# Optimization experiments

Hardware: AMD Instinct MI355X
Metric: run time of the kernel (lower is better)

Reference implementation:

```python
import jax, jax.numpy as jnp
import numpy as np

MUL0, MUL1 = 128, 64            # scalar (0e) and vector (1o) multiplicities
B = 8192                        # batch of nodes
SQRT3 = 3.0 ** 0.5
SQRT6 = 6.0 ** 0.5

# path normalization (e3nn 'component' irrep norm / 'element' path norm):
# coeff_ins = sqrt(dim(ir_out) / fan_in(i_out)), fan_in = sum_{ins -> i_out} mul1*mul2
A_0E = (1.0 / (MUL0 * MUL0 + MUL1 * MUL1)) ** 0.5   # paths (0,0,0)+(1,1,0)
A_1O = (3.0 / (MUL0 * MUL1 + MUL1 * MUL0)) ** 0.5   # paths (0,1,1)+(1,0,1)
A_1E = (3.0 / (MUL1 * MUL1)) ** 0.5                  # path  (1,1,1)


def _levi_civita():
    eps = np.zeros((3, 3, 3), dtype=np.float32)
    eps[0, 1, 2] = eps[1, 2, 0] = eps[2, 0, 1] = 1.0
    eps[0, 2, 1] = eps[2, 1, 0] = eps[1, 0, 2] = -1.0
    return jnp.asarray(eps)


def setup_inputs() -> dict:
    key = jax.random.key(0)
    ks = jax.random.split(key, 7)
    return {
        "x1": jax.random.normal(ks[0], (B, MUL0 + 3 * MUL1), dtype=jnp.float32),
        "x2": jax.random.normal(ks[1], (B, MUL0 + 3 * MUL1), dtype=jnp.float32),
        "w000": jax.random.normal(ks[2], (MUL0, MUL0, MUL0), dtype=jnp.float32),
        "w011": jax.random.normal(ks[3], (MUL0, MUL1, MUL1), dtype=jnp.float32),
        "w101": jax.random.normal(ks[4], (MUL1, MUL0, MUL1), dtype=jnp.float32),
        "w110": jax.random.normal(ks[5], (MUL1, MUL1, MUL0), dtype=jnp.float32),
        "w111": jax.random.normal(ks[6], (MUL1, MUL1, MUL1), dtype=jnp.float32),
    }


def reference(x1, x2, w000, w011, w101, w110, w111):
    b = x1.shape[0]
    # split irreps: scalars [b, 128], vectors [b, 64, 3]
    s1, v1 = x1[:, :MUL0], x1[:, MUL0:].reshape(b, MUL1, 3)
    s2, v2 = x2[:, :MUL0], x2[:, MUL0:].reshape(b, MUL1, 3)

    # 0e output: 0e x 0e -> 0e (w3j = 1) and 1o x 1o -> 0e (w3j = delta/sqrt3)
    out0 = A_0E * (
        jnp.einsum("uvw,bu,bv->bw", w000, s1, s2)
        + jnp.einsum("uvw,bui,bvi->bw", w110, v1, v2) / SQRT3
    )

    # 1o output: 0e x 1o -> 1o and 1o x 0e -> 1o (w3j = delta/sqrt3)
    out1o = (A_1O / SQRT3) * (
        jnp.einsum("uvw,bu,bvi->bwi", w011, s1, v2)
        + jnp.einsum("uvw,bui,bv->bwi", w101, v1, s2)
    )

    # 1e output: 1o x 1o -> 1e (w3j = levi-civita / sqrt6)
    eps = _levi_civita()
    out1e = (A_1E / SQRT6) * jnp.einsum("uvw,bui,bvj,ijk->bwk", w111, v1, v2, eps)

    return jnp.concatenate(
        [out0, out1o.reshape(b, -1), out1e.reshape(b, -1)], axis=-1
    )  # [b, 128 + 192 + 192] = [b, 512]
```

## Files before the change

kernel.cpp:

```cpp
#include <hip/hip_runtime.h>
#include <stdint.h>


typedef _Float16 f16;
typedef f16 f16x8 __attribute__((ext_vector_type(8)));
typedef float f32x4 __attribute__((ext_vector_type(4)));
typedef int i32x4 __attribute__((ext_vector_type(4)));

#define OFF_W000 0u
#define OFF_W110 2097152u
#define OFF_W011 2621440u
#define OFF_W101 3145728u
#define OFF_W111 3670016u
#define OFF_XS1  3932160u
#define OFF_XS2  4980736u
#define OFF_XV1  6029312u
#define OFF_XV2  7602176u
#define OFF_S0A  9175040u
#define OFF_S0B  10223616u
#define OFF_S1O  13369344u
#define WS_ELEMS 14942208u

#define SC_0E 0.006987712429686843f
#define SC_1O 0.0078125f
#define SC_1E 0.011048543456039806f

__global__ void tile_all_k(const float* __restrict__ w000, const float* __restrict__ w011,
                           const float* __restrict__ w101, const float* __restrict__ w110,
                           const float* __restrict__ w111, const float* __restrict__ x1,
                           const float* __restrict__ x2, f16* __restrict__ ws)
{
  unsigned tid = blockIdx.x*256u + threadIdx.x;
  if (tid < 2097152u) {
    unsigned e=tid&7u, n=(tid>>3)&63u, q=(tid>>9)&3u, p=(tid>>11)&1u,
             u=(tid>>12)&127u, vh=(tid>>19)&1u, h=(tid>>20)&1u;
    unsigned v = vh*64u + p*32u + q*8u + e;
    ws[OFF_W000+tid] = (f16)w000[u*16384u + v*128u + h*64u + n];
    return;
  }
  tid -= 2097152u;
  if (tid < 524288u) {
    unsigned e=tid&7u, n=(tid>>3)&63u, q=(tid>>9)&3u, p=(tid>>11)&1u,
             u=(tid>>12)&63u, h=(tid>>18)&1u;
    unsigned v = p*32u + q*8u + e;
    ws[OFF_W110+tid] = (f16)(w110[u*8192u + v*128u + h*64u + n] * 0.5773502691896258f);
    return;
  }
  tid -= 524288u;
  if (tid < 524288u) {
    unsigned e=tid&7u, n=(tid>>3)&63u, q=(tid>>9)&3u, p=(tid>>11)&1u, u=tid>>12;
    unsigned v = p*32u + q*8u + e;
    ws[OFF_W011+tid] = (f16)w011[u*4096u + v*64u + n];
    return;
  }
  tid -= 524288u;
  if (tid < 524288u) {
    unsigned e=tid&7u, n=(tid>>3)&63u, q=(tid>>9)&3u, p=(tid>>11)&1u, u=tid>>12;
    unsigned v = p*32u + q*8u + e;
    ws[OFF_W101+tid] = (f16)w101[v*8192u + u*64u + n];
    return;
  }
  tid -= 524288u;
  if (tid < 262144u) {
    unsigned e=tid&7u, n=(tid>>3)&63u, q=(tid>>9)&3u, p=(tid>>11)&1u, u=tid>>12;
    unsigned v = p*32u + q*8u + e;
    ws[OFF_W111+tid] = (f16)w111[u*4096u + v*64u + n];
    return;
  }
  tid -= 262144u;
  if (tid < 1048576u) {
    unsigned e=tid&7u, r=(tid>>3)&127u, uo=(tid>>10)&15u, rt=tid>>14;
    ws[OFF_XS1+tid] = (f16)x1[(rt*128u+r)*320u + uo*8u + e];
    return;
  }
  tid -= 1048576u;
  if (tid < 1572864u) {
    unsigned e=tid&7u, r=(tid>>3)&127u, ov=(tid>>10)&7u, rest=tid>>13;
    unsigned i=rest%3u, rt=rest/3u;
    ws[OFF_XV1+tid] = (f16)x1[(rt*128u+r)*320u + 128u + (ov*8u+e)*3u + i];
    return;
  }
  tid -= 1572864u;
  if (tid < 1048576u) {
    unsigned e=tid&7u, r=(tid>>3)&127u, uo=(tid>>10)&15u, rt=tid>>14;
    ws[OFF_XS2+tid] = (f16)x2[(rt*128u+r)*320u + uo*8u + e];
    return;
  }
  tid -= 1048576u;
  {
    unsigned e=tid&7u, r=(tid>>3)&127u, ov=(tid>>10)&7u, rest=tid>>13;
    unsigned i=rest%3u, rt=rest/3u;
    ws[OFF_XV2+tid] = (f16)x2[(rt*128u+r)*320u + 128u + (ov*8u+e)*3u + i];
  }
}

#define GLD16(g,l) __builtin_amdgcn_global_load_lds( \
    (const __attribute__((address_space(1))) unsigned int*)(g), \
    (__attribute__((address_space(3))) unsigned int*)(l), 16, 0, 0)

#define WAITV(n) asm volatile("s_waitcnt vmcnt(" #n ")" ::: "memory")

template<bool NEG, int SS>
__device__ __forceinline__ void run_phase(const f16* __restrict__ Wt,
    const f16* __restrict__ aW, const f16* __restrict__ bW, int bRow,
    f16* sWw, f16* sAw, f32x4 (&acc)[4][4], int lane)
{
  constexpr int M = SS*8;
  const int q = lane >> 4, r15 = lane & 15;

  f16x8 br[4][2];
#pragma unroll
  for (int mt=0; mt<4; ++mt)
#pragma unroll
    for (int o=0; o<2; ++o)
      br[mt][o] = *(const f16x8*)(bW + (o*4+q)*1024 + (bRow + mt*16 + r15)*8);
#pragma unroll
  for (int mt=0; mt<4; ++mt)
#pragma unroll
    for (int o=0; o<2; ++o) {
      i32x4 tmp = __builtin_bit_cast(i32x4, br[mt][o]);
      asm volatile("" :: "v"(tmp));
    }

  auto stPair = [&](int p, int slot){
    const char* s = (const char*)Wt + (size_t)p*8192;
    char* d = (char*)sWw + slot*8192;
#pragma unroll
    for (int c=0; c<8; ++c)
      GLD16(s + c*1024 + lane*16, d + c*1024);
  };
  auto stA = [&](int ss2){
    GLD16((const char*)(aW + ss2*1024) + lane*16, (char*)sAw + (ss2&1)*1024);
  };

  stPair(0,0); stA(0); stPair(1,1);

  f16x8 aR[4];
#pragma unroll 1
  for (int ss = 0; ss < SS; ++ss) {
#pragma unroll
    for (int kc = 0; kc < 8; ++kc) {
      const int t = ss*8 + kc;
      if (kc == 7) { if (ss+1 < SS) { WAITV(9); } else { WAITV(0); } }
      else         { WAITV(8); }
      if (kc == 0) {
#pragma unroll
        for (int mt=0; mt<4; ++mt)
          aR[mt] = *(const f16x8*)(sAw + (ss&1)*512 + (mt*16+r15)*8);
      }
      __builtin_amdgcn_s_setprio(1);
#pragma unroll
      for (int p=0; p<2; ++p) {
        f16x8 af[4];
#pragma unroll
        for (int mt=0; mt<4; ++mt) {
          f16 av = aR[mt][kc];
          if constexpr (NEG) av = -av;
          af[mt] = av * br[mt][p];
        }
#pragma unroll
        for (int nt=0; nt<4; ++nt) {
          f16x8 bw = *(const f16x8*)(sWw + (kc&1)*4096 + p*2048 + (q*64 + nt*16 + r15)*8);
#pragma unroll
          for (int mt=0; mt<4; ++mt)
            acc[mt][nt] = __builtin_amdgcn_mfma_f32_16x16x32_f16(af[mt], bw, acc[mt][nt], 0,0,0);
        }
      }
      __builtin_amdgcn_s_setprio(0);
      __builtin_amdgcn_sched_barrier(0);
      if (kc == 6 && ss+1 < SS) stA(ss+1);
      if (t + 2 < M) stPair(t+2, kc&1);
    }
  }
}

__global__ __launch_bounds__(256, 2)
void tp_main(f16* __restrict__ ws, float* __restrict__ out)
{
  __shared__ f16 smem[36864];
  const int lane = threadIdx.x & 63, wid = threadIdx.x >> 6;
  f16* sWw = smem + wid*8192;
  f16* sAw = smem + 32768 + wid*1024;
  const int q = lane >> 4, r15 = lane & 15;
  const int sub = wid >> 1, rh = wid & 1;

  f32x4 acc[4][4];
#pragma unroll
  for (int a=0;a<4;++a)
#pragma unroll
    for (int b=0;b<4;++b) acc[a][b] = (f32x4){0.f,0.f,0.f,0.f};

  const int bid = blockIdx.x;

#define STORE_DIRECT(base_col_expr, SC)                                   \
  _Pragma("unroll")                                                       \
  for (int mt=0;mt<4;++mt)                                                \
    _Pragma("unroll")                                                     \
    for (int nt=0;nt<4;++nt)                                              \
      _Pragma("unroll")                                                   \
      for (int rg=0;rg<4;++rg)                                            \
        out[(rowb+mt*16+q*4+rg)*512 + (base_col_expr)] = (SC)*acc[mt][nt][rg];

#define STORE_SLAB(slab, stride, col_expr, SC)                            \
  _Pragma("unroll")                                                       \
  for (int mt=0;mt<4;++mt)                                                \
    _Pragma("unroll")                                                     \
    for (int nt=0;nt<4;++nt)                                              \
      _Pragma("unroll")                                                   \
      for (int rg=0;rg<4;++rg)                                            \
        (slab)[(rowb+mt*16+q*4+rg)*(stride) + (col_expr)] = (f16)((SC)*acc[mt][nt][rg]);

  if (bid < 128) {
    const int rtp = bid >> 2, vh = (bid >> 1) & 1, h = bid & 1;
    const int rtt = rtp*2 + sub;
    const f16* aW = ws + OFF_XS1 + rtt*16384 + rh*512;
    const f16* bW = ws + OFF_XS2 + rtt*16384 + vh*8192;
    const f16* Wt = ws + OFF_W000 + h*1048576u + vh*524288u;
    run_phase<false,16>(Wt, aW, bW, rh*64, sWw, sAw, acc, lane);
    const int rowb = rtt*128 + rh*64;
    if (vh == 0) { STORE_DIRECT(h*64+nt*16+r15, SC_0E) }
    else { f16* slab = ws + OFF_S0A; STORE_SLAB(slab, 128, h*64+nt*16+r15, SC_0E) }
  } else if (bid < 224) {
    const int id = bid-128, i = id%3, rtp = id/3;
    const int rtt = rtp*2 + sub;
    const f16* aW = ws + OFF_XS1 + rtt*16384 + rh*512;
    const f16* bW = ws + OFF_XV2 + (rtt*3+i)*8192;
    run_phase<false,16>(ws + OFF_W011, aW, bW, rh*64, sWw, sAw, acc, lane);
    const int rowb = rtt*128 + rh*64;
    STORE_DIRECT(128 + 3*(nt*16+r15) + i, SC_1O)
  } else if (bid < 320) {
    const int id = bid-224, i = id%3, rtp = id/3;
    const int rtt = rtp*2 + sub;
    const f16* aW = ws + OFF_XS2 + rtt*16384 + rh*512;
    const f16* bW = ws + OFF_XV1 + (rtt*3+i)*8192;
    run_phase<false,16>(ws + OFF_W101, aW, bW, rh*64, sWw, sAw, acc, lane);
    const int rowb = rtt*128 + rh*64;
    f16* slab = ws + OFF_S1O;
    STORE_SLAB(slab, 192, 3*(nt*16+r15) + i, SC_1O)
  } else if (bid < 416) {
    const int id = bid-320, kk = id%3, rtp = id/3;
    int i = kk+1; if (i>2) i-=3;
    int j = kk+2; if (j>2) j-=3;
    const int rtt = rtp*2 + sub;
    run_phase<false,8>(ws + OFF_W111,
        ws + OFF_XV1 + (rtt*3+i)*8192 + rh*512, ws + OFF_XV2 + (rtt*3+j)*8192,
        rh*64, sWw, sAw, acc, lane);
    run_phase<true,8>(ws + OFF_W111,
        ws + OFF_XV1 + (rtt*3+j)*8192 + rh*512, ws + OFF_XV2 + (rtt*3+i)*8192,
        rh*64, sWw, sAw, acc, lane);
    const int rowb = rtt*128 + rh*64;
    STORE_DIRECT(320 + 3*(nt*16+r15) + kk, SC_1E)
  } else {
    const int id = bid-416, i = id%3, h = (id/3)&1, rtp = id/6;
    const int rtt = rtp*2 + sub;
    const f16* aW = ws + OFF_XV1 + (rtt*3+i)*8192 + rh*512;
    const f16* bW = ws + OFF_XV2 + (rtt*3+i)*8192;
    run_phase<false,8>(ws + OFF_W110 + h*262144u, aW, bW, rh*64, sWw, sAw, acc, lane);
    const int rowb = rtt*128 + rh*64;
    f16* slab = ws + OFF_S0B + (unsigned)i*1048576u;
    STORE_SLAB(slab, 128, h*64+nt*16+r15, SC_0E)
  }
#undef STORE_DIRECT
#undef STORE_SLAB
}

__global__ void ep_add(const f16* __restrict__ ws, float* __restrict__ out)
{
  unsigned tid = blockIdx.x*256u + threadIdx.x;
  if (tid < 1048576u) {
    unsigned r = tid>>7, c = tid&127u;
    float s = (float)ws[OFF_S0A+tid] + (float)ws[OFF_S0B+tid]
            + (float)ws[OFF_S0B+1048576u+tid] + (float)ws[OFF_S0B+2097152u+tid];
    out[r*512u+c] += s;
  } else {
    unsigned t2 = tid - 1048576u;
    unsigned r = t2/192u, c = t2 - r*192u;
    out[r*512u+128u+c] += (float)ws[OFF_S1O+t2];
  }
}

extern "C" void kernel_launch(void* const* d_in, const int* in_sizes, int n_in,
                              void* d_out, int out_size, void* d_ws, size_t ws_size,
                              hipStream_t stream)
{
  const float* x1   = (const float*)d_in[0];
  const float* x2   = (const float*)d_in[1];
  const float* w000 = (const float*)d_in[2];
  const float* w011 = (const float*)d_in[3];
  const float* w101 = (const float*)d_in[4];
  const float* w110 = (const float*)d_in[5];
  const float* w111 = (const float*)d_in[6];
  float* out = (float*)d_out;
  f16* ws   = (f16*)d_ws;

  if (ws_size < (size_t)WS_ELEMS * 2) return;

  tile_all_k<<<35840, 256, 0, stream>>>(w000, w011, w101, w110, w111, x1, x2, ws);
  tp_main<<<608, 256, 0, stream>>>(ws, out);
  ep_add<<<10240, 256, 0, stream>>>(ws, out);
}
```

Baseline: 157.6 us.

## Share weight tiles across waves in LDS and split N across waves

Before, each wave streamed its own private copy of the weight tile into LDS. Now the four waves of a block load a shared weight tile cooperatively, with each wave staging a quarter of it and using a 4-slot ring with block barriers. Each block now covers one 128-row tile, with waves split by row half and N half, and the accumulators shrink to 4x2. Lower LDS and register use allows 4 blocks per CU, and the grid grows to 1024 blocks with a remapped job order. In exchange this adds a workgroup barrier every k-step and halves per-wave reuse of the A fragments.

```diff
diff --git a/kernel.cpp b/kernel.cpp
--- a/kernel.cpp
+++ b/kernel.cpp
@@ -102,11 +102,13 @@
 
 template<bool NEG, int SS>
 __device__ __forceinline__ void run_phase(const f16* __restrict__ Wt,
-    const f16* __restrict__ aW, const f16* __restrict__ bW, int bRow,
-    f16* sWw, f16* sAw, f32x4 (&acc)[4][4], int lane)
+    const f16* __restrict__ aW, const f16* __restrict__ bW, int bRow, int nh,
+    f16* sW, f16* sAw, f32x4 (&acc)[4][2], int lane, int wid)
 {
   constexpr int M = SS*8;
   const int q = lane >> 4, r15 = lane & 15;
+
+  WAITV(0);
 
   f16x8 br[4][2];
 #pragma unroll
@@ -123,17 +125,16 @@
     }
 
   auto stPair = [&](int p, int slot){
-    const char* s = (const char*)Wt + (size_t)p*8192;
-    char* d = (char*)sWw + slot*8192;
-#pragma unroll
-    for (int c=0; c<8; ++c)
-      GLD16(s + c*1024 + lane*16, d + c*1024);
+    const char* s = (const char*)Wt + p*8192 + wid*2048 + lane*16;
+    char* d = (char*)sW + slot*8192 + wid*2048;
+    GLD16(s, d);
+    GLD16(s + 1024, d + 1024);
   };
   auto stA = [&](int ss2){
     GLD16((const char*)(aW + ss2*1024) + lane*16, (char*)sAw + (ss2&1)*1024);
   };
 
-  stPair(0,0); stA(0); stPair(1,1);
+  stA(0); stPair(0,0); stPair(1,1); stPair(2,2);
 
   f16x8 aR[4];
 #pragma unroll 1
@@ -141,8 +142,13 @@
 #pragma unroll
     for (int kc = 0; kc < 8; ++kc) {
       const int t = ss*8 + kc;
-      if (kc == 7) { if (ss+1 < SS) { WAITV(9); } else { WAITV(0); } }
-      else         { WAITV(8); }
+      if (kc == 7)      { if (ss+1 < SS) { WAITV(5); } else { WAITV(0); } }
+      else if (kc == 6) { if (ss+1 < SS) { WAITV(4); } else { WAITV(2); } }
+      else              { WAITV(4); }
+      __builtin_amdgcn_s_barrier();
+      __builtin_amdgcn_sched_barrier(0);
+      if (kc == 6 && ss+1 < SS) stA(ss+1);
+      if (t + 3 < M) stPair(t+3, (kc+3)&3);
       if (kc == 0) {
 #pragma unroll
         for (int mt=0; mt<4; ++mt)
@@ -159,106 +165,110 @@
           af[mt] = av * br[mt][p];
         }
 #pragma unroll
-        for (int nt=0; nt<4; ++nt) {
-          f16x8 bw = *(const f16x8*)(sWw + (kc&1)*4096 + p*2048 + (q*64 + nt*16 + r15)*8);
+        for (int nt=0; nt<2; ++nt) {
+          f16x8 bw = *(const f16x8*)(sW + (kc&3)*4096 + p*2048 + q*512
+                                     + (nh*32 + nt*16 + r15)*8);
 #pragma unroll
           for (int mt=0; mt<4; ++mt)
             acc[mt][nt] = __builtin_amdgcn_mfma_f32_16x16x32_f16(af[mt], bw, acc[mt][nt], 0,0,0);
         }
       }
       __builtin_amdgcn_s_setprio(0);
-      __builtin_amdgcn_sched_barrier(0);
-      if (kc == 6 && ss+1 < SS) stA(ss+1);
-      if (t + 2 < M) stPair(t+2, kc&1);
     }
   }
-}
-
-__global__ __launch_bounds__(256, 2)
+  __builtin_amdgcn_s_barrier();
+  __builtin_amdgcn_sched_barrier(0);
+}
+
+__global__ __launch_bounds__(256, 4)
 void tp_main(f16* __restrict__ ws, float* __restrict__ out)
 {
-  __shared__ f16 smem[36864];
+  __shared__ f16 smem[20480];
+  f16* sW = smem;
   const int lane = threadIdx.x & 63, wid = threadIdx.x >> 6;
-  f16* sWw = smem + wid*8192;
-  f16* sAw = smem + 32768 + wid*1024;
+  f16* sAw = smem + 16384 + wid*1024;
   const int q = lane >> 4, r15 = lane & 15;
-  const int sub = wid >> 1, rh = wid & 1;
-
-  f32x4 acc[4][4];
+  const int rh = wid & 1, nh = wid >> 1;
+
+  f32x4 acc[4][2];
 #pragma unroll
   for (int a=0;a<4;++a)
 #pragma unroll
-    for (int b=0;b<4;++b) acc[a][b] = (f32x4){0.f,0.f,0.f,0.f};
-
-  const int bid = blockIdx.x;
-
-#define STORE_DIRECT(base_col_expr, SC)                                   \
+    for (int b=0;b<2;++b) acc[a][b] = (f32x4){0.f,0.f,0.f,0.f};
+
+  const int jid = (blockIdx.x & 7)*128 + (blockIdx.x >> 3);
+
+#define STORE_DIRECT(col_expr, SC)                                        \
   _Pragma("unroll")                                                       \
   for (int mt=0;mt<4;++mt)                                                \
     _Pragma("unroll")                                                     \
-    for (int nt=0;nt<4;++nt)                                              \
+    for (int nt=0;nt<2;++nt)                                              \
       _Pragma("unroll")                                                   \
       for (int rg=0;rg<4;++rg)                                            \
-        out[(rowb+mt*16+q*4+rg)*512 + (base_col_expr)] = (SC)*acc[mt][nt][rg];
+        out[(rowb+mt*16+q*4+rg)*512 + (col_expr)] = (SC)*acc[mt][nt][rg];
 
 #define STORE_SLAB(slab, stride, col_expr, SC)                            \
   _Pragma("unroll")                                                       \
   for (int mt=0;mt<4;++mt)                                                \
     _Pragma("unroll")                                                     \
-    for (int nt=0;nt<4;++nt)                                              \
+    for (int nt=0;nt<2;++nt)                                              \
       _Pragma("unroll")                                                   \
       for (int rg=0;rg<4;++rg)                                            \
         (slab)[(rowb+mt*16+q*4+rg)*(stride) + (col_expr)] = (f16)((SC)*acc[mt][nt][rg]);
 
-  if (bid < 128) {
-    const int rtp = bid >> 2, vh = (bid >> 1) & 1, h = bid & 1;
-    const int rtt = rtp*2 + sub;
-    const f16* aW = ws + OFF_XS1 + rtt*16384 + rh*512;
-    const f16* bW = ws + OFF_XS2 + rtt*16384 + vh*8192;
+  if (jid < 256) {
+    const int quarter = jid >> 6, rt = jid & 63;
+    const int h = quarter & 1, vh = quarter >> 1;
+    const f16* aW = ws + OFF_XS1 + rt*16384 + rh*512;
+    const f16* bW = ws + OFF_XS2 + rt*16384 + vh*8192;
     const f16* Wt = ws + OFF_W000 + h*1048576u + vh*524288u;
-    run_phase<false,16>(Wt, aW, bW, rh*64, sWw, sAw, acc, lane);
-    const int rowb = rtt*128 + rh*64;
-    if (vh == 0) { STORE_DIRECT(h*64+nt*16+r15, SC_0E) }
-    else { f16* slab = ws + OFF_S0A; STORE_SLAB(slab, 128, h*64+nt*16+r15, SC_0E) }
-  } else if (bid < 224) {
-    const int id = bid-128, i = id%3, rtp = id/3;
-    const int rtt = rtp*2 + sub;
-    const f16* aW = ws + OFF_XS1 + rtt*16384 + rh*512;
-    const f16* bW = ws + OFF_XV2 + (rtt*3+i)*8192;
-    run_phase<false,16>(ws + OFF_W011, aW, bW, rh*64, sWw, sAw, acc, lane);
-    const int rowb = rtt*128 + rh*64;
-    STORE_DIRECT(128 + 3*(nt*16+r15) + i, SC_1O)
-  } else if (bid < 320) {
-    const int id = bid-224, i = id%3, rtp = id/3;
-    const int rtt = rtp*2 + sub;
-    const f16* aW = ws + OFF_XS2 + rtt*16384 + rh*512;
-    const f16* bW = ws + OFF_XV1 + (rtt*3+i)*8192;
-    run_phase<false,16>(ws + OFF_W101, aW, bW, rh*64, sWw, sAw, acc, lane);
-    const int rowb = rtt*128 + rh*64;
+    run_phase<false,16>(Wt, aW, bW, rh*64, nh, sW, sAw, acc, lane, wid);
+    const int rowb = rt*128 + rh*64;
+    if (vh == 0) { STORE_DIRECT(h*64 + nh*32 + nt*16 + r15, SC_0E) }
+    else { f16* slab = ws + OFF_S0A; STORE_SLAB(slab, 128, h*64 + nh*32 + nt*16 + r15, SC_0E) }
+  } else if (jid < 448) {
+    const int s = jid-256, i = s>>6, rt = s&63;
+    const f16* aW = ws + OFF_XS1 + rt*16384 + rh*512;
+    const f16* bW = ws + OFF_XV2 + (rt*3+i)*8192;
+    run_phase<false,16>(ws + OFF_W011, aW, bW, rh*64, nh, sW, sAw, acc, lane, wid);
+    const int rowb = rt*128 + rh*64;
+    STORE_DIRECT(128 + 3*(nh*32 + nt*16 + r15) + i, SC_1O)
+  } else if (jid < 640) {
+    const int s = jid-448, i = s>>6, rt = s&63;
+    const f16* aW = ws + OFF_XS2 + rt*16384 + rh*512;
+    const f16* bW = ws + OFF_XV1 + (rt*3+i)*8192;
+    run_phase<false,16>(ws + OFF_W101, aW, bW, rh*64, nh, sW, sAw, acc, lane, wid);
+    const int rowb = rt*128 + rh*64;
     f16* slab = ws + OFF_S1O;
-    STORE_SLAB(slab, 192, 3*(nt*16+r15) + i, SC_1O)
-  } else if (bid < 416) {
-    const int id = bid-320, kk = id%3, rtp = id/3;
+    STORE_SLAB(slab, 192, 3*(nh*32 + nt*16 + r15) + i, SC_1O)
+  } else if (jid < 832) {
+    const int s = jid-640, kk = s>>6, rt = s&63;
     int i = kk+1; if (i>2) i-=3;
     int j = kk+2; if (j>2) j-=3;
-    const int rtt = rtp*2 + sub;
     run_phase<false,8>(ws + OFF_W111,
-        ws + OFF_XV1 + (rtt*3+i)*8192 + rh*512, ws + OFF_XV2 + (rtt*3+j)*8192,
-        rh*64, sWw, sAw, acc, lane);
+        ws + OFF_XV1 + (rt*3+i)*8192 + rh*512, ws + OFF_XV2 + (rt*3+j)*8192,
+        rh*64, nh, sW, sAw, acc, lane, wid);
     run_phase<true,8>(ws + OFF_W111,
-        ws + OFF_XV1 + (rtt*3+j)*8192 + rh*512, ws + OFF_XV2 + (rtt*3+i)*8192,
-        rh*64, sWw, sAw, acc, lane);
-    const int rowb = rtt*128 + rh*64;
-    STORE_DIRECT(320 + 3*(nt*16+r15) + kk, SC_1E)
+        ws + OFF_XV1 + (rt*3+j)*8192 + rh*512, ws + OFF_XV2 + (rt*3+i)*8192,
+        rh*64, nh, sW, sAw, acc, lane, wid);
+    const int rowb = rt*128 + rh*64;
+    STORE_DIRECT(320 + 3*(nh*32 + nt*16 + r15) + kk, SC_1E)
   } else {
-    const int id = bid-416, i = id%3, h = (id/3)&1, rtp = id/6;
-    const int rtt = rtp*2 + sub;
-    const f16* aW = ws + OFF_XV1 + (rtt*3+i)*8192 + rh*512;
-    const f16* bW = ws + OFF_XV2 + (rtt*3+i)*8192;
-    run_phase<false,8>(ws + OFF_W110 + h*262144u, aW, bW, rh*64, sWw, sAw, acc, lane);
-    const int rowb = rtt*128 + rh*64;
+    const int s = jid-832, i = s>>6, rt = s&63;
+    const f16* aW = ws + OFF_XV1 + (rt*3+i)*8192 + rh*512;
+    const f16* bW = ws + OFF_XV2 + (rt*3+i)*8192;
+    const int rowb = rt*128 + rh*64;
     f16* slab = ws + OFF_S0B + (unsigned)i*1048576u;
-    STORE_SLAB(slab, 128, h*64+nt*16+r15, SC_0E)
+#pragma unroll 1
+    for (int h = 0; h < 2; ++h) {
+      run_phase<false,8>(ws + OFF_W110 + (unsigned)h*262144u, aW, bW, rh*64, nh,
+                         sW, sAw, acc, lane, wid);
+      STORE_SLAB(slab, 128, h*64 + nh*32 + nt*16 + r15, SC_0E)
+#pragma unroll
+      for (int a=0;a<4;++a)
+#pragma unroll
+        for (int b=0;b<2;++b) acc[a][b] = (f32x4){0.f,0.f,0.f,0.f};
+    }
   }
 #undef STORE_DIRECT
 #undef STORE_SLAB
@@ -296,6 +306,6 @@
   if (ws_size < (size_t)WS_ELEMS * 2) return;
 
   tile_all_k<<<35840, 256, 0, stream>>>(w000, w011, w101, w110, w111, x1, x2, ws);
-  tp_main<<<608, 256, 0, stream>>>(ws, out);
+  tp_main<<<1024, 256, 0, stream>>>(ws, out);
   ep_add<<<10240, 256, 0, stream>>>(ws, out);
 }
```

Result: slower. 165.0 us (+4.7%).

## Restructure tensor-product GEMMs into single-wave 32x32 MFMA jobs with split-K partials

Applied to the files above, without the earlier changes.

Replaces 4-wave 256-thread blocks running 16x16x32 MFMAs with 2048 single-wavefront blocks using 32x32x16 MFMAs, each computing a 128-row by 64-column tile over a half-K slice. The weight and activation staging layouts are re-tiled to match, with a 4-slot LDS pipeline and more split-K partial slabs. The epilogue becomes a row-major pass that sums up to six f16 partials per output. This aims to raise parallelism and MFMA efficiency and to balance work across CUs, at the cost of a larger workspace, more f16 partial traffic and reduction work in ep_add, and less intra-block reuse.

```diff
diff --git a/kernel.cpp b/kernel.cpp
--- a/kernel.cpp
+++ b/kernel.cpp
@@ -4,7 +4,7 @@
 
 typedef _Float16 f16;
 typedef f16 f16x8 __attribute__((ext_vector_type(8)));
-typedef float f32x4 __attribute__((ext_vector_type(4)));
+typedef float f32x16 __attribute__((ext_vector_type(16)));
 typedef int i32x4 __attribute__((ext_vector_type(4)));
 
 #define OFF_W000 0u
@@ -16,10 +16,10 @@
 #define OFF_XS2  4980736u
 #define OFF_XV1  6029312u
 #define OFF_XV2  7602176u
-#define OFF_S0A  9175040u
-#define OFF_S0B  10223616u
-#define OFF_S1O  13369344u
-#define WS_ELEMS 14942208u
+#define OFF_S0   9175040u
+#define OFF_S1   15466496u
+#define OFF_S2   20185088u
+#define WS_ELEMS 21757952u
 
 #define SC_0E 0.006987712429686843f
 #define SC_1O 0.0078125f
@@ -32,65 +32,77 @@
 {
   unsigned tid = blockIdx.x*256u + threadIdx.x;
   if (tid < 2097152u) {
-    unsigned e=tid&7u, n=(tid>>3)&63u, q=(tid>>9)&3u, p=(tid>>11)&1u,
-             u=(tid>>12)&127u, vh=(tid>>19)&1u, h=(tid>>20)&1u;
-    unsigned v = vh*64u + p*32u + q*8u + e;
-    ws[OFF_W000+tid] = (f16)w000[u*16384u + v*128u + h*64u + n];
+    unsigned e=tid&7u, col=(tid>>3)&31u, hf=(tid>>8)&1u, kk=(tid>>9)&1u,
+             ct=(tid>>10)&1u, t=(tid>>11)&127u, q=tid>>18;
+    unsigned h=q&1u, uh=(q>>1)&1u, vh=q>>2;
+    unsigned u = uh*64u + (t>>1);
+    unsigned v = vh*64u + (t&1u)*32u + kk*16u + hf*8u + e;
+    unsigned n = h*64u + ct*32u + col;
+    ws[OFF_W000+tid] = (f16)w000[u*16384u + v*128u + n];
     return;
   }
   tid -= 2097152u;
   if (tid < 524288u) {
-    unsigned e=tid&7u, n=(tid>>3)&63u, q=(tid>>9)&3u, p=(tid>>11)&1u,
-             u=(tid>>12)&63u, h=(tid>>18)&1u;
-    unsigned v = p*32u + q*8u + e;
-    ws[OFF_W110+tid] = (f16)(w110[u*8192u + v*128u + h*64u + n] * 0.5773502691896258f);
+    unsigned e=tid&7u, col=(tid>>3)&31u, hf=(tid>>8)&1u, kk=(tid>>9)&1u,
+             ct=(tid>>10)&1u, t=(tid>>11)&127u, h=tid>>18;
+    unsigned u = t>>1;
+    unsigned v = (t&1u)*32u + kk*16u + hf*8u + e;
+    unsigned n = h*64u + ct*32u + col;
+    ws[OFF_W110+tid] = (f16)(w110[u*8192u + v*128u + n] * 0.5773502691896258f);
     return;
   }
   tid -= 524288u;
   if (tid < 524288u) {
-    unsigned e=tid&7u, n=(tid>>3)&63u, q=(tid>>9)&3u, p=(tid>>11)&1u, u=tid>>12;
-    unsigned v = p*32u + q*8u + e;
+    unsigned e=tid&7u, col=(tid>>3)&31u, hf=(tid>>8)&1u, kk=(tid>>9)&1u,
+             ct=(tid>>10)&1u, t=(tid>>11)&127u, uh=tid>>18;
+    unsigned u = uh*64u + (t>>1);
+    unsigned v = (t&1u)*32u + kk*16u + hf*8u + e;
+    unsigned n = ct*32u + col;
     ws[OFF_W011+tid] = (f16)w011[u*4096u + v*64u + n];
     return;
   }
   tid -= 524288u;
   if (tid < 524288u) {
-    unsigned e=tid&7u, n=(tid>>3)&63u, q=(tid>>9)&3u, p=(tid>>11)&1u, u=tid>>12;
-    unsigned v = p*32u + q*8u + e;
+    unsigned e=tid&7u, col=(tid>>3)&31u, hf=(tid>>8)&1u, kk=(tid>>9)&1u,
+             ct=(tid>>10)&1u, t=(tid>>11)&127u, uh=tid>>18;
+    unsigned u = uh*64u + (t>>1);
+    unsigned v = (t&1u)*32u + kk*16u + hf*8u + e;
+    unsigned n = ct*32u + col;
     ws[OFF_W101+tid] = (f16)w101[v*8192u + u*64u + n];
     return;
   }
   tid -= 524288u;
   if (tid < 262144u) {
-    unsigned e=tid&7u, n=(tid>>3)&63u, q=(tid>>9)&3u, p=(tid>>11)&1u, u=tid>>12;
-    unsigned v = p*32u + q*8u + e;
+    unsigned e=tid&7u, col=(tid>>3)&31u, hf=(tid>>8)&1u, kk=(tid>>9)&1u,
+             ct=(tid>>10)&1u, t=tid>>11;
+    unsigned u = t>>1;
+    unsigned v = (t&1u)*32u + kk*16u + hf*8u + e;
+    unsigned n = ct*32u + col;
     ws[OFF_W111+tid] = (f16)w111[u*4096u + v*64u + n];
     return;
   }
   tid -= 262144u;
   if (tid < 1048576u) {
-    unsigned e=tid&7u, r=(tid>>3)&127u, uo=(tid>>10)&15u, rt=tid>>14;
-    ws[OFF_XS1+tid] = (f16)x1[(rt*128u+r)*320u + uo*8u + e];
+    unsigned e=tid&7u, r=(tid>>3)&8191u, o=tid>>16;
+    ws[OFF_XS1+tid] = (f16)x1[r*320u + o*8u + e];
+    return;
+  }
+  tid -= 1048576u;
+  if (tid < 1048576u) {
+    unsigned e=tid&7u, r=(tid>>3)&8191u, o=tid>>16;
+    ws[OFF_XS2+tid] = (f16)x2[r*320u + o*8u + e];
     return;
   }
   tid -= 1048576u;
   if (tid < 1572864u) {
-    unsigned e=tid&7u, r=(tid>>3)&127u, ov=(tid>>10)&7u, rest=tid>>13;
-    unsigned i=rest%3u, rt=rest/3u;
-    ws[OFF_XV1+tid] = (f16)x1[(rt*128u+r)*320u + 128u + (ov*8u+e)*3u + i];
+    unsigned e=tid&7u, r=(tid>>3)&8191u, o=(tid>>16)&7u, i=tid>>19;
+    ws[OFF_XV1+tid] = (f16)x1[r*320u + 128u + (o*8u+e)*3u + i];
     return;
   }
   tid -= 1572864u;
-  if (tid < 1048576u) {
-    unsigned e=tid&7u, r=(tid>>3)&127u, uo=(tid>>10)&15u, rt=tid>>14;
-    ws[OFF_XS2+tid] = (f16)x2[(rt*128u+r)*320u + uo*8u + e];
-    return;
-  }
-  tid -= 1048576u;
   {
-    unsigned e=tid&7u, r=(tid>>3)&127u, ov=(tid>>10)&7u, rest=tid>>13;
-    unsigned i=rest%3u, rt=rest/3u;
-    ws[OFF_XV2+tid] = (f16)x2[(rt*128u+r)*320u + 128u + (ov*8u+e)*3u + i];
+    unsigned e=tid&7u, r=(tid>>3)&8191u, o=(tid>>16)&7u, i=tid>>19;
+    ws[OFF_XV2+tid] = (f16)x2[r*320u + 128u + (o*8u+e)*3u + i];
   }
 }
 
@@ -99,184 +111,209 @@
     (__attribute__((address_space(3))) unsigned int*)(l), 16, 0, 0)
 
 #define WAITV(n) asm volatile("s_waitcnt vmcnt(" #n ")" ::: "memory")
-
-template<bool NEG, int SS>
-__device__ __forceinline__ void run_phase(const f16* __restrict__ Wt,
-    const f16* __restrict__ aW, const f16* __restrict__ bW, int bRow,
-    f16* sWw, f16* sAw, f32x4 (&acc)[4][4], int lane)
-{
-  constexpr int M = SS*8;
-  const int q = lane >> 4, r15 = lane & 15;
-
-  f16x8 br[4][2];
-#pragma unroll
-  for (int mt=0; mt<4; ++mt)
-#pragma unroll
-    for (int o=0; o<2; ++o)
-      br[mt][o] = *(const f16x8*)(bW + (o*4+q)*1024 + (bRow + mt*16 + r15)*8);
-#pragma unroll
-  for (int mt=0; mt<4; ++mt)
-#pragma unroll
-    for (int o=0; o<2; ++o) {
-      i32x4 tmp = __builtin_bit_cast(i32x4, br[mt][o]);
-      asm volatile("" :: "v"(tmp));
-    }
-
-  auto stPair = [&](int p, int slot){
-    const char* s = (const char*)Wt + (size_t)p*8192;
-    char* d = (char*)sWw + slot*8192;
-#pragma unroll
-    for (int c=0; c<8; ++c)
-      GLD16(s + c*1024 + lane*16, d + c*1024);
+#define SBAR0 __builtin_amdgcn_sched_barrier(0)
+
+__device__ __forceinline__ void run_phase(
+    const f16* __restrict__ Wq, const f16* __restrict__ aPl, int uob,
+    const f16* __restrict__ bPl, int ob, int rowb,
+    f16* sW, f16* sA, int lane, f32x16 (&acc)[4][2])
+{
+  const int l31 = lane & 31, hf = lane >> 5;
+  constexpr int SS = 8;
+
+  WAITV(0);
+  f16x8 br[4][2][2];
+#pragma unroll
+  for (int rt=0; rt<4; ++rt)
+#pragma unroll
+    for (int vh=0; vh<2; ++vh)
+#pragma unroll
+      for (int kk=0; kk<2; ++kk)
+        br[rt][vh][kk] = *(const f16x8*)(bPl +
+            ((unsigned)(ob + vh*4 + kk*2 + hf)*8192u + (unsigned)(rowb + rt*32 + l31))*8u);
+#pragma unroll
+  for (int rt=0; rt<4; ++rt)
+#pragma unroll
+    for (int vh=0; vh<2; ++vh)
+#pragma unroll
+      for (int kk=0; kk<2; ++kk) {
+        i32x4 tmp = __builtin_bit_cast(i32x4, br[rt][vh][kk]);
+        asm volatile("" :: "v"(tmp));
+      }
+
+  const char* Ws = (const char*)Wq + lane*16;
+  auto stage = [&](int t, int slot){
+    const char* s = Ws + t*4096;
+    char* d = (char*)sW + slot*4096;
+    GLD16(s,      d);
+    GLD16(s+1024, d+1024);
+    GLD16(s+2048, d+2048);
+    GLD16(s+3072, d+3072);
   };
+  const char* As = (const char*)aPl + (size_t)uob*131072 + (size_t)rowb*16 + lane*16;
   auto stA = [&](int ss2){
-    GLD16((const char*)(aW + ss2*1024) + lane*16, (char*)sAw + (ss2&1)*1024);
+    const char* s = As + ss2*131072;
+    char* d = (char*)sA + (ss2&1)*2048;
+    GLD16(s,      d);
+    GLD16(s+1024, d+1024);
   };
 
-  stPair(0,0); stA(0); stPair(1,1);
+  stA(0); stage(0,0); stage(1,1); stage(2,2);
 
   f16x8 aR[4];
 #pragma unroll 1
-  for (int ss = 0; ss < SS; ++ss) {
-#pragma unroll
-    for (int kc = 0; kc < 8; ++kc) {
-      const int t = ss*8 + kc;
-      if (kc == 7) { if (ss+1 < SS) { WAITV(9); } else { WAITV(0); } }
-      else         { WAITV(8); }
-      if (kc == 0) {
-#pragma unroll
-        for (int mt=0; mt<4; ++mt)
-          aR[mt] = *(const f16x8*)(sAw + (ss&1)*512 + (mt*16+r15)*8);
+  for (int ss=0; ss<SS; ++ss) {
+#pragma unroll
+    for (int kc=0; kc<16; ++kc) {
+      if (kc==14)      { if (ss==SS-1) { WAITV(4); } else { WAITV(10); } }
+      else if (kc==15) { if (ss==SS-1) { WAITV(0); } else { WAITV(10); } }
+      else             { WAITV(8); }
+      SBAR0;
+      if (kc==13 && ss<SS-1) stA(ss+1);
+      if (kc<13 || ss<SS-1) stage(ss*16+kc+3, (kc+3)&3);
+      if (kc==0) {
+#pragma unroll
+        for (int rt=0; rt<4; ++rt)
+          aR[rt] = *(const f16x8*)(sA + (ss&1)*1024 + (rt*32+l31)*8);
       }
+      const f16* Wl = sW + (kc&3)*2048;
       __builtin_amdgcn_s_setprio(1);
 #pragma unroll
-      for (int p=0; p<2; ++p) {
+      for (int kk=0; kk<2; ++kk) {
         f16x8 af[4];
 #pragma unroll
-        for (int mt=0; mt<4; ++mt) {
-          f16 av = aR[mt][kc];
-          if constexpr (NEG) av = -av;
-          af[mt] = av * br[mt][p];
+        for (int rt=0; rt<4; ++rt) {
+          f16 av = aR[rt][kc>>1];
+          af[rt] = av * br[rt][kc&1][kk];
         }
 #pragma unroll
-        for (int nt=0; nt<4; ++nt) {
-          f16x8 bw = *(const f16x8*)(sWw + (kc&1)*4096 + p*2048 + (q*64 + nt*16 + r15)*8);
-#pragma unroll
-          for (int mt=0; mt<4; ++mt)
-            acc[mt][nt] = __builtin_amdgcn_mfma_f32_16x16x32_f16(af[mt], bw, acc[mt][nt], 0,0,0);
+        for (int ct=0; ct<2; ++ct) {
+          f16x8 bw = *(const f16x8*)(Wl + (ct*2+kk)*512 + hf*256 + l31*8);
+#pragma unroll
+          for (int rt=0; rt<4; ++rt)
+            acc[rt][ct] = __builtin_amdgcn_mfma_f32_32x32x16_f16(af[rt], bw, acc[rt][ct], 0,0,0);
         }
       }
       __builtin_amdgcn_s_setprio(0);
-      __builtin_amdgcn_sched_barrier(0);
-      if (kc == 6 && ss+1 < SS) stA(ss+1);
-      if (t + 2 < M) stPair(t+2, kc&1);
     }
   }
 }
 
-__global__ __launch_bounds__(256, 2)
+__global__ __launch_bounds__(64, 2)
 void tp_main(f16* __restrict__ ws, float* __restrict__ out)
 {
-  __shared__ f16 smem[36864];
-  const int lane = threadIdx.x & 63, wid = threadIdx.x >> 6;
-  f16* sWw = smem + wid*8192;
-  f16* sAw = smem + 32768 + wid*1024;
-  const int q = lane >> 4, r15 = lane & 15;
-  const int sub = wid >> 1, rh = wid & 1;
-
-  f32x4 acc[4][4];
-#pragma unroll
-  for (int a=0;a<4;++a)
-#pragma unroll
-    for (int b=0;b<4;++b) acc[a][b] = (f32x4){0.f,0.f,0.f,0.f};
+  __shared__ f16 smem[10240];
+  f16* sW = smem;
+  f16* sA = smem + 8192;
+  const int lane = threadIdx.x & 63;
+  const int l31 = lane & 31, hf = lane >> 5;
+
+  f32x16 acc[4][2];
+#pragma unroll
+  for (int a=0; a<4; ++a)
+#pragma unroll
+    for (int b=0; b<2; ++b)
+#pragma unroll
+      for (int r=0; r<16; ++r) acc[a][b][r] = 0.f;
 
   const int bid = blockIdx.x;
-
-#define STORE_DIRECT(base_col_expr, SC)                                   \
-  _Pragma("unroll")                                                       \
-  for (int mt=0;mt<4;++mt)                                                \
-    _Pragma("unroll")                                                     \
-    for (int nt=0;nt<4;++nt)                                              \
-      _Pragma("unroll")                                                   \
-      for (int rg=0;rg<4;++rg)                                            \
-        out[(rowb+mt*16+q*4+rg)*512 + (base_col_expr)] = (SC)*acc[mt][nt][rg];
-
-#define STORE_SLAB(slab, stride, col_expr, SC)                            \
-  _Pragma("unroll")                                                       \
-  for (int mt=0;mt<4;++mt)                                                \
-    _Pragma("unroll")                                                     \
-    for (int nt=0;nt<4;++nt)                                              \
-      _Pragma("unroll")                                                   \
-      for (int rg=0;rg<4;++rg)                                            \
-        (slab)[(rowb+mt*16+q*4+rg)*(stride) + (col_expr)] = (f16)((SC)*acc[mt][nt][rg]);
-
-  if (bid < 128) {
-    const int rtp = bid >> 2, vh = (bid >> 1) & 1, h = bid & 1;
-    const int rtt = rtp*2 + sub;
-    const f16* aW = ws + OFF_XS1 + rtt*16384 + rh*512;
-    const f16* bW = ws + OFF_XS2 + rtt*16384 + vh*8192;
-    const f16* Wt = ws + OFF_W000 + h*1048576u + vh*524288u;
-    run_phase<false,16>(Wt, aW, bW, rh*64, sWw, sAw, acc, lane);
-    const int rowb = rtt*128 + rh*64;
-    if (vh == 0) { STORE_DIRECT(h*64+nt*16+r15, SC_0E) }
-    else { f16* slab = ws + OFF_S0A; STORE_SLAB(slab, 128, h*64+nt*16+r15, SC_0E) }
-  } else if (bid < 224) {
-    const int id = bid-128, i = id%3, rtp = id/3;
-    const int rtt = rtp*2 + sub;
-    const f16* aW = ws + OFF_XS1 + rtt*16384 + rh*512;
-    const f16* bW = ws + OFF_XV2 + (rtt*3+i)*8192;
-    run_phase<false,16>(ws + OFF_W011, aW, bW, rh*64, sWw, sAw, acc, lane);
-    const int rowb = rtt*128 + rh*64;
-    STORE_DIRECT(128 + 3*(nt*16+r15) + i, SC_1O)
-  } else if (bid < 320) {
-    const int id = bid-224, i = id%3, rtp = id/3;
-    const int rtt = rtp*2 + sub;
-    const f16* aW = ws + OFF_XS2 + rtt*16384 + rh*512;
-    const f16* bW = ws + OFF_XV1 + (rtt*3+i)*8192;
-    run_phase<false,16>(ws + OFF_W101, aW, bW, rh*64, sWw, sAw, acc, lane);
-    const int rowb = rtt*128 + rh*64;
-    f16* slab = ws + OFF_S1O;
-    STORE_SLAB(slab, 192, 3*(nt*16+r15) + i, SC_1O)
-  } else if (bid < 416) {
-    const int id = bid-320, kk = id%3, rtp = id/3;
+  const int jid = (bid&7)*256 + (bid>>3);
+
+  const f16 *Wq, *aPl, *bPl;
+  int uob=0, ob=0, rowb, cbase=0, cmul=1;
+  unsigned sbase=0; bool direct; float sc;
+
+  if (jid < 512) {
+    int rt = jid & 63, q = jid >> 6;
+    int h = q&1, uh = (q>>1)&1, vh = q>>2;
+    Wq  = ws + OFF_W000 + (unsigned)q*262144u;
+    aPl = ws + OFF_XS1;  uob = uh*8;
+    bPl = ws + OFF_XS2;  ob  = vh*8;
+    rowb = rt*128; sc = SC_0E;
+    direct = (vh==0 && uh==0);
+    cbase = h*64; cmul = 1;
+    sbase = OFF_S0 + (unsigned)(((vh*2+uh-1)*2 + h))*524288u;
+  } else if (jid < 896) {
+    int s = jid-512, rt = s&63, g = s>>6, i = g%3, h = g/3;
+    Wq  = ws + OFF_W110 + (unsigned)h*262144u;
+    aPl = ws + OFF_XV1 + (unsigned)i*524288u;
+    bPl = ws + OFF_XV2 + (unsigned)i*524288u;
+    rowb = rt*128; sc = SC_0E; direct = false;
+    sbase = OFF_S0 + (unsigned)((3+i)*2 + h)*524288u;
+  } else if (jid < 1280) {
+    int s = jid-896, rt = s&63, g = s>>6, i = g%3, uh = g/3;
+    Wq  = ws + OFF_W011 + (unsigned)uh*262144u;
+    aPl = ws + OFF_XS1;  uob = uh*8;
+    bPl = ws + OFF_XV2 + (unsigned)i*524288u;
+    rowb = rt*128; sc = SC_1O;
+    direct = (uh==0); cbase = 128+i; cmul = 3;
+    sbase = OFF_S1 + (unsigned)i*524288u;
+  } else if (jid < 1664) {
+    int s = jid-1280, rt = s&63, g = s>>6, i = g%3, uh = g/3;
+    Wq  = ws + OFF_W101 + (unsigned)uh*262144u;
+    aPl = ws + OFF_XS2;  uob = uh*8;
+    bPl = ws + OFF_XV1 + (unsigned)i*524288u;
+    rowb = rt*128; sc = SC_1O; direct = false;
+    sbase = OFF_S1 + (unsigned)((1+uh)*3 + i)*524288u;
+  } else {
+    int s = jid-1664, rt = s&63, g = s>>6, kk = g%3, sg = g/3;
     int i = kk+1; if (i>2) i-=3;
     int j = kk+2; if (j>2) j-=3;
-    const int rtt = rtp*2 + sub;
-    run_phase<false,8>(ws + OFF_W111,
-        ws + OFF_XV1 + (rtt*3+i)*8192 + rh*512, ws + OFF_XV2 + (rtt*3+j)*8192,
-        rh*64, sWw, sAw, acc, lane);
-    run_phase<true,8>(ws + OFF_W111,
-        ws + OFF_XV1 + (rtt*3+j)*8192 + rh*512, ws + OFF_XV2 + (rtt*3+i)*8192,
-        rh*64, sWw, sAw, acc, lane);
-    const int rowb = rtt*128 + rh*64;
-    STORE_DIRECT(320 + 3*(nt*16+r15) + kk, SC_1E)
+    Wq = ws + OFF_W111;
+    if (sg==0) { aPl = ws + OFF_XV1 + (unsigned)i*524288u; bPl = ws + OFF_XV2 + (unsigned)j*524288u; }
+    else       { aPl = ws + OFF_XV1 + (unsigned)j*524288u; bPl = ws + OFF_XV2 + (unsigned)i*524288u; }
+    rowb = rt*128; sc = (sg==0) ? SC_1E : -SC_1E;
+    direct = (sg==0); cbase = 320+kk; cmul = 3;
+    sbase = OFF_S2 + (unsigned)kk*524288u;
+  }
+
+  run_phase(Wq, aPl, uob, bPl, ob, rowb, sW, sA, lane, acc);
+
+  if (direct) {
+#pragma unroll
+    for (int rt=0; rt<4; ++rt)
+#pragma unroll
+      for (int ct=0; ct<2; ++ct)
+#pragma unroll
+        for (int rg=0; rg<16; ++rg) {
+          int row = (rg&3) + 8*(rg>>2) + 4*hf;
+          out[(unsigned)(rowb + rt*32 + row)*512u + (unsigned)(cbase + cmul*(ct*32 + l31))]
+              = sc * acc[rt][ct][rg];
+        }
   } else {
-    const int id = bid-416, i = id%3, h = (id/3)&1, rtp = id/6;
-    const int rtt = rtp*2 + sub;
-    const f16* aW = ws + OFF_XV1 + (rtt*3+i)*8192 + rh*512;
-    const f16* bW = ws + OFF_XV2 + (rtt*3+i)*8192;
-    run_phase<false,8>(ws + OFF_W110 + h*262144u, aW, bW, rh*64, sWw, sAw, acc, lane);
-    const int rowb = rtt*128 + rh*64;
-    f16* slab = ws + OFF_S0B + (unsigned)i*1048576u;
-    STORE_SLAB(slab, 128, h*64+nt*16+r15, SC_0E)
-  }
-#undef STORE_DIRECT
-#undef STORE_SLAB
+#pragma unroll
+    for (int rt=0; rt<4; ++rt)
+#pragma unroll
+      for (int ct=0; ct<2; ++ct)
+#pragma unroll
+        for (int rg=0; rg<16; ++rg) {
+          int row = (rg&3) + 8*(rg>>2) + 4*hf;
+          ws[sbase + (unsigned)(rowb + rt*32 + row)*64u + (unsigned)(ct*32 + l31)]
+              = (f16)(sc * acc[rt][ct][rg]);
+        }
+  }
 }
 
 __global__ void ep_add(const f16* __restrict__ ws, float* __restrict__ out)
 {
   unsigned tid = blockIdx.x*256u + threadIdx.x;
-  if (tid < 1048576u) {
-    unsigned r = tid>>7, c = tid&127u;
-    float s = (float)ws[OFF_S0A+tid] + (float)ws[OFF_S0B+tid]
-            + (float)ws[OFF_S0B+1048576u+tid] + (float)ws[OFF_S0B+2097152u+tid];
-    out[r*512u+c] += s;
+  unsigned r = tid >> 9, c = tid & 511u;
+  float s = 0.f;
+  if (c < 128u) {
+    unsigned h = c>>6, cc = c&63u;
+#pragma unroll
+    for (int j=0; j<6; ++j)
+      s += (float)ws[OFF_S0 + ((unsigned)(j*2)+h)*524288u + r*64u + cc];
+  } else if (c < 320u) {
+    unsigned t = c-128u, n = (t*21846u)>>16, i = t - n*3u;
+#pragma unroll
+    for (int j=0; j<3; ++j)
+      s += (float)ws[OFF_S1 + ((unsigned)j*3u+i)*524288u + r*64u + n];
   } else {
-    unsigned t2 = tid - 1048576u;
-    unsigned r = t2/192u, c = t2 - r*192u;
-    out[r*512u+128u+c] += (float)ws[OFF_S1O+t2];
-  }
+    unsigned t = c-320u, n = (t*21846u)>>16, kk = t - n*3u;
+    s = (float)ws[OFF_S2 + kk*524288u + r*64u + n];
+  }
+  out[tid] += s;
 }
 
 extern "C" void kernel_launch(void* const* d_in, const int* in_sizes, int n_in,
@@ -296,6 +333,6 @@
   if (ws_size < (size_t)WS_ELEMS * 2) return;
 
   tile_all_k<<<35840, 256, 0, stream>>>(w000, w011, w101, w110, w111, x1, x2, ws);
-  tp_main<<<608, 256, 0, stream>>>(ws, out);
-  ep_add<<<10240, 256, 0, stream>>>(ws, out);
-}
+  tp_main<<<2048, 64, 0, stream>>>(ws, out);
+  ep_add<<<16384, 256, 0, stream>>>(ws, out);
+}
```

Result: slower. 167.8 us (+6.5%).
